# Kernel tuning notes

Hardware: AMD Instinct MI355X
Metric: run time of the kernel (lower is better)

## Reference

```python
import jax, jax.numpy as jnp
import numpy as np

N, H, B = 4096, 128, 32
K_MSG, K_INT = 32, 20
CUTOFFS = (3.0, 3.0, 6.0, 6.0, 10.0, 10.0)  # two EGNN layers per backbone
silu = jax.nn.silu


def _lin(key, fi, fo):
    s = 1.0 / np.sqrt(fi)
    return jax.random.uniform(key, (fi, fo), jnp.float32, -s, s)


def setup_inputs():
    ks = jax.random.split(jax.random.key(0), 16)
    L = 6

    def stack(k, fi, fo):
        return jnp.stack([_lin(kk, fi, fo) for kk in jax.random.split(k, L)])

    return dict(
        h=jax.random.normal(ks[0], (N, H), jnp.float32),
        pos=3.0 * jax.random.normal(ks[1], (N, 3), jnp.float32),
        batch=jnp.sort(jax.random.randint(ks[2], (N,), 0, B)),
        edge_w1=stack(ks[3], 2 * H + 1, H), edge_b1=jnp.zeros((L, H)),
        edge_w2=stack(ks[4], H, H), edge_b2=jnp.zeros((L, H)),
        coord_w1=stack(ks[5], H, H), coord_b1=jnp.zeros((L, H)),
        coord_w2=stack(ks[6], H, 1),
        node_w1=stack(ks[7], 2 * H, H), node_b1=jnp.zeros((L, H)),
        node_w2=stack(ks[8], H, H), node_b2=jnp.zeros((L, H)),
        fw1=_lin(ks[9], H, 128), fb1=jnp.zeros((128,)),
        fw2=_lin(ks[10], 128, 3), fb2=jnp.zeros((3,)),
        iw=jnp.stack([_lin(kk, 2 * H + 2, 1) for kk in jax.random.split(ks[11], 3)]),
        ib=jnp.zeros((3, 1)),
        cw1=_lin(ks[12], H, 128), cb1=jnp.zeros((128,)),
        cw2=_lin(ks[13], 128, 64), cb2=jnp.zeros((64,)),
        sw=_lin(ks[14], H, 1), sb=jnp.zeros((1,)),
    )


def _neighbors(pos, batch, cutoff, k):
    # radius graph with fixed fan-out: k nearest same-graph neighbors within cutoff
    p = jax.lax.stop_gradient(pos)
    d2 = jnp.sum((p[:, None, :] - p[None, :, :]) ** 2, -1)  # [N,N]
    valid = (batch[:, None] == batch[None, :]) & (~jnp.eye(p.shape[0], dtype=bool)) & (d2 <= cutoff * cutoff)
    neg, idx = jax.lax.top_k(jnp.where(valid, -d2, -jnp.inf), k)
    return idx, neg > -jnp.inf  # [N,k] int, [N,k] bool validity mask


def _egnn_layer(h, pos, idx, mask, ew1, eb1, ew2, eb2, cw1, cb1, cw2, nw1, nb1, nw2, nb2):
    mf = mask[..., None].astype(h.dtype)  # [N,K,1]
    hj = h[idx]                            # [N,K,H] gather
    rel = pos[:, None, :] - pos[idx]       # [N,K,3]
    d2 = jnp.sum(rel * rel, -1, keepdims=True)
    hi = jnp.broadcast_to(h[:, None, :], hj.shape)
    m = silu(jnp.concatenate([hi, hj, d2], -1) @ ew1 + eb1)
    m = silu(m @ ew2 + eb2) * mf           # masked messages [N,K,H]
    c = silu(m @ cw1 + cb1) @ cw2          # per-edge coord weight [N,K,1]
    cnt = jnp.maximum(jnp.sum(mf, 1), 1.0)
    pos = pos + jnp.sum(rel * c * mf, 1) / cnt
    h = h + (silu(jnp.concatenate([h, jnp.sum(m, 1)], -1) @ nw1 + nb1) @ nw2 + nb2)
    return h, pos


def _forward(h, pos, batch, edge_w1, edge_b1, edge_w2, edge_b2, coord_w1, coord_b1, coord_w2,
             node_w1, node_b1, node_w2, node_b2, fw1, fb1, fw2, fb2, iw, ib, cw1, cb1, cw2, cb2, sw, sb):
    idx = mask = None
    for l in range(6):  # short(3.0) x2, medium(6.0) x2, long(10.0) x2
        if l % 2 == 0:
            idx, mask = _neighbors(pos, batch, CUTOFFS[l], K_MSG)
        h, pos = _egnn_layer(h, pos, idx, mask, edge_w1[l], edge_b1[l], edge_w2[l], edge_b2[l],
                             coord_w1[l], coord_b1[l], coord_w2[l],
                             node_w1[l], node_b1[l], node_w2[l], node_b2[l])
    forces = jnp.tanh(h @ fw1 + fb1) @ fw2 + fb2
    # interaction detection: radius graph (r=10, max 20 neighbors)
    iidx, imask = _neighbors(pos, batch, 10.0, K_INT)
    rel = pos[:, None, :] - pos[iidx]
    dist = jnp.sqrt(jnp.sum(rel * rel, -1, keepdims=True) + 1e-12)  # [N,K,1]
    hi = jnp.broadcast_to(h[:, None, :], (h.shape[0], K_INT, h.shape[1]))
    feats = jnp.concatenate([hi, h[iidx], dist, dist / 10.0], -1)  # [N,K,2H+2]
    scores = jax.nn.sigmoid(jnp.einsum('nkf,tfo->tnko', feats, iw) + ib[:, None, None, :])
    scores = scores * imask[None, :, :, None].astype(h.dtype)  # zero padded edges
    conformer = jax.nn.relu(h @ cw1 + cb1) @ cw2 + cb2
    steric = h @ sw + sb
    return h, pos, forces, scores[0], scores[1], scores[2], conformer, steric


def reference(h, pos, batch, edge_w1, edge_b1, edge_w2, edge_b2, coord_w1, coord_b1, coord_w2,
              node_w1, node_b1, node_w2, node_b2, fw1, fb1, fw2, fb2, iw, ib, cw1, cb1, cw2, cb2, sw, sb):
    return _forward(h, pos, batch, edge_w1, edge_b1, edge_w2, edge_b2, coord_w1, coord_b1, coord_w2,
                    node_w1, node_b1, node_w2, node_b2, fw1, fb1, fw2, fb2, iw, ib, cw1, cb1, cw2, cb2, sw, sb)
```

## Files before the change

### kernel.cpp

```cpp
#include <hip/hip_runtime.h>
#include <hip/hip_bf16.h>

#define NN 4096
#define HD 128
#define KE 32
#define KI 20
#define XLD 132
#define PLOF 68

#define OFF_H   0
#define OFF_POS 524288
#define OFF_F   536576
#define OFF_S   548864
#define OFF_C   794624
#define OFF_ST  1056768

typedef unsigned short u16;
typedef unsigned int u32;
typedef unsigned long long u64;
typedef __attribute__((ext_vector_type(8))) short bf16x8;
typedef __attribute__((ext_vector_type(4))) float f32x4;

__device__ __forceinline__ float b2f(u16 u) {
  union { u32 i; float f; } c; c.i = ((u32)u) << 16; return c.f;
}
__device__ __forceinline__ float silu_f(float x) { return x / (1.f + __expf(-x)); }
__device__ __forceinline__ void stout(void* out, int fp32m, size_t i, float v) {
  if (fp32m) ((float*)out)[i] = v;
  else ((__hip_bfloat16*)out)[i] = __float2bfloat16(v);
}
__device__ __forceinline__ u32 f2b(float f) {
  u32 u = __float_as_uint(f);
  return (u + 0x7fffu + ((u >> 16) & 1u)) >> 16;
}
__device__ __forceinline__ void packplane(float a, float b, u32& H, u32& L) {
  asm("v_cvt_pk_bf16_f32 %0, %1, %2" : "=v"(H) : "v"(a), "v"(b));
  float hfa = __uint_as_float(H << 16);
  float hfb = __uint_as_float(H & 0xffff0000u);
  asm("v_cvt_pk_bf16_f32 %0, %1, %2" : "=v"(L) : "v"(a - hfa), "v"(b - hfb));
}

__global__ void probe_dtype(const u16* __restrict__ h, int* __restrict__ flag) {
  if (threadIdx.x == 0) atomicExch(flag, 0);
  __syncthreads();
  int bad = 0;
  for (int i = threadIdx.x; i < 8192; i += 256) {
    float v = b2f(h[i]);
    if (!(v > -1000.f && v < 1000.f)) bad = 1;
  }
  if (bad) atomicOr(flag, 1);
}

struct CvtTable {
  const void* src[25];
  int dstoff[25];
  int cnt[25];
};

__global__ void convert_all(CvtTable tab, float* __restrict__ wsf, const int* __restrict__ flag) {
  const int seg = blockIdx.y;
  const int i = blockIdx.x * 256 + threadIdx.x;
  if (i >= tab.cnt[seg]) return;
  float v;
  if (*flag) v = ((const float*)tab.src[seg])[i];
  else       v = b2f(((const u16*)tab.src[seg])[i]);
  wsf[tab.dstoff[seg] + i] = v;
}

__global__ void pack_weights(const float* __restrict__ wsf, int offEW1, int offEW2, int offCW1,
                             u16* __restrict__ WBP) {
  int tid = blockIdx.x * 256 + threadIdx.x;
  if (tid >= 18 * 32768) return;
  int m = tid >> 15;
  int rix = tid & 32767;
  int layer = m / 3, s = m % 3;
  const float* src;
  if (s == 0)      src = wsf + offEW1 + (size_t)layer * 257 * HD + 128 * HD;
  else if (s == 1) src = wsf + offEW2 + (size_t)layer * HD * HD;
  else             src = wsf + offCW1 + (size_t)layer * HD * HD;
  int jh = rix & 15, lane = (rix >> 4) & 63, ot = (rix >> 10) & 7, kt = rix >> 13;
  int j = jh & 7;
  int f = kt * 32 + (lane >> 4) * 8 + j;
  int o = ot * 16 + (lane & 15);
  float v = src[f * HD + o];
  u32 hb = f2b(v);
  float hf = __uint_as_float(hb << 16);
  u32 lb = f2b(v - hf);
  WBP[tid] = (jh < 8) ? (u16)hb : (u16)lb;
}

__global__ void graph_bounds(const int* __restrict__ batch, int* __restrict__ gstart) {
  int n = blockIdx.x * 256 + threadIdx.x;
  if (n >= NN) return;
  int v = batch[n];
  int pv = (n == 0) ? -1 : batch[n - 1];
  for (int b = pv + 1; b <= v; b++) gstart[b] = n;
  if (n == NN - 1) for (int b = v + 1; b <= 32; b++) gstart[b] = NN;
}

__global__ __launch_bounds__(256) void neigh_kernel(
    const float* __restrict__ pos, const int* __restrict__ batch,
    const int* __restrict__ gstart, int* __restrict__ idx, int* __restrict__ cnt,
    int Ksel, float cut2) {
  const int lane = threadIdx.x & 63;
  const int i = blockIdx.x * 4 + (threadIdx.x >> 6);
  const int b = batch[i];
  const int gs = gstart[b];
  const int ge = gstart[b + 1];
  const int span = ge - gs;
  const float px = pos[i * 3 + 0], py = pos[i * 3 + 1], pz = pos[i * 3 + 2];
  u64 key[16];
#pragma unroll
  for (int tq = 0; tq < 16; tq++) {
    u64 k64 = ~0ull;
    if (tq * 64 < span) {
      int j = gs + tq * 64 + lane;
      if (j < ge && j != i) {
        float dx = px - pos[j * 3 + 0];
        float dy = py - pos[j * 3 + 1];
        float dz = pz - pos[j * 3 + 2];
        float d2 = dx * dx + dy * dy + dz * dz;
        if (d2 <= cut2) k64 = (((u64)__float_as_uint(d2)) << 32) | (u32)j;
      }
    }
    key[tq] = k64;
  }
  u64 thresh = 0;
  int myidx = i;
  int mycnt = 0;
  for (int s = 0; s < Ksel; s++) {
    u64 m = ~0ull;
#pragma unroll
    for (int tq = 0; tq < 16; tq++) {
      if (tq * 64 < span) {
        u64 kk = key[tq];
        if (kk >= thresh && kk < m) m = kk;
      }
    }
    for (int off = 32; off > 0; off >>= 1) {
      u64 o = __shfl_down(m, (unsigned)off, 64);
      if (o < m) m = o;
    }
    m = __shfl(m, 0, 64);
    if (m != ~0ull) {
      if (lane == s) myidx = (int)(m & 0xffffffffu);
      mycnt++;
      thresh = m + 1;
    } else break;
  }
  if (lane < Ksel) idx[i * Ksel + lane] = myidx;
  if (lane == 0) cnt[i] = mycnt;
}

__device__ __forceinline__ void mfma_stageS(const u32* xp_, const u16* __restrict__ WP,
                                            int w, int lane, int nt0, int nt1,
                                            f32x4 acc[4]) {
  const int l16 = lane & 15, q = lane >> 4;
  f32x4 z = {0.f, 0.f, 0.f, 0.f};
  acc[0] = z; acc[1] = z; acc[2] = z; acc[3] = z;
#pragma unroll
  for (int kt = 0; kt < 4; kt++) {
    const u16* wb = WP + (size_t)((kt * 8 + w) * 64 + lane) * 16;
    bf16x8 wh = *(const bf16x8*)(wb);
    bf16x8 wl = *(const bf16x8*)(wb + 8);
#pragma unroll
    for (int Et = 0; Et < 4; Et++) {
      if ((Et < 2) ? (Et < nt0) : (Et - 2 < nt1)) {
        const u32* xr = xp_ + (Et * 16 + l16) * XLD + kt * 16 + q * 4;
        bf16x8 xh = *(const bf16x8*)(xr);
        bf16x8 xl = *(const bf16x8*)(xr + PLOF);
        acc[Et] = __builtin_amdgcn_mfma_f32_16x16x32_bf16(wh, xl, acc[Et], 0, 0, 0);
        acc[Et] = __builtin_amdgcn_mfma_f32_16x16x32_bf16(wl, xh, acc[Et], 0, 0, 0);
        acc[Et] = __builtin_amdgcn_mfma_f32_16x16x32_bf16(wh, xh, acc[Et], 0, 0, 0);
      }
    }
  }
}

__global__ __launch_bounds__(512, 4) void egnn_layer(
    const float* __restrict__ h_in, const float* __restrict__ pos_in,
    float* __restrict__ h_out, float* __restrict__ pos_out,
    const int* __restrict__ idx, const int* __restrict__ cnt,
    const float* __restrict__ ew1, const float* __restrict__ eb1,
    const float* __restrict__ eb2,
    const float* __restrict__ cb1, const float* __restrict__ cw2,
    const float* __restrict__ nw1, const float* __restrict__ nb1,
    const float* __restrict__ nw2, const float* __restrict__ nb2,
    const u16* __restrict__ wbp) {
  __shared__ __align__(16) u32 xp[64 * XLD];
  __shared__ float hi_s[2][HD], hpart_s[2][HD], msum_s[2][HD], u_s[2][HD];
  __shared__ float red_s[512];
  __shared__ float ce_red[64][8];
  __shared__ float rel_s[3][64], d2_s[64], mf_s[64], ce_s[64];
  __shared__ int idx_s[64], cn_s[2];

  const int t = threadIdx.x;
  const int i0 = blockIdx.x * 2;
  const int lane = t & 63;
  const int w = __builtin_amdgcn_readfirstlane(t >> 6);
  const int l16 = lane & 15, q = lane >> 4;

  if (t < 64) idx_s[t] = idx[(size_t)(i0 + (t >> 5)) * KE + (t & 31)];
  else if (t < 66) cn_s[t - 64] = cnt[i0 + (t - 64)];
  if (t >= 256) {
    const int nt = t - 256;
    hi_s[nt >> 7][nt & 127] = h_in[(size_t)(i0 + (nt >> 7)) * HD + (nt & 127)];
  }
  __syncthreads();

  const int nt0 = __builtin_amdgcn_readfirstlane((cn_s[0] + 15) >> 4);
  const int nt1 = __builtin_amdgcn_readfirstlane((cn_s[1] + 15) >> 4);

  if (t < 64) {
    const int nd = t >> 5, ic = i0 + nd;
    const int j = idx_s[t];
    const float rx = pos_in[ic * 3 + 0] - pos_in[j * 3 + 0];
    const float ry = pos_in[ic * 3 + 1] - pos_in[j * 3 + 1];
    const float rz = pos_in[ic * 3 + 2] - pos_in[j * 3 + 2];
    rel_s[0][t] = rx; rel_s[1][t] = ry; rel_s[2][t] = rz;
    d2_s[t] = rx * rx + ry * ry + rz * rz;
    mf_s[t] = ((t & 31) < cn_s[nd]) ? 1.0f : 0.0f;
  }
  {
    const int ge_ = t & 63;
    const int myEt = ge_ >> 4;
    const bool glive = (myEt < 2) ? (myEt < nt0) : (myEt - 2 < nt1);
    if (glive) {
      const int j = idx_s[ge_];
      const int f0 = (t >> 6) * 16;
      const float4* src = (const float4*)(h_in + (size_t)j * HD + f0);
      float4 v0 = src[0], v1 = src[1], v2 = src[2], v3 = src[3];
      u32 H0, L0, H1, L1, H2, L2, H3, L3, H4, L4, H5, L5, H6, L6, H7, L7;
      packplane(v0.x, v0.y, H0, L0); packplane(v0.z, v0.w, H1, L1);
      packplane(v1.x, v1.y, H2, L2); packplane(v1.z, v1.w, H3, L3);
      packplane(v2.x, v2.y, H4, L4); packplane(v2.z, v2.w, H5, L5);
      packplane(v3.x, v3.y, H6, L6); packplane(v3.z, v3.w, H7, L7);
      u32* dh = xp + ge_ * XLD + (f0 >> 1);
      uint4 a; a.x = H0; a.y = H1; a.z = H2; a.w = H3;
      uint4 b; b.x = H4; b.y = H5; b.z = H6; b.w = H7;
      uint4 c; c.x = L0; c.y = L1; c.z = L2; c.w = L3;
      uint4 d; d.x = L4; d.y = L5; d.z = L6; d.w = L7;
      *(uint4*)(dh) = a;            *(uint4*)(dh + 4) = b;
      *(uint4*)(dh + PLOF) = c;     *(uint4*)(dh + PLOF + 4) = d;
    }
  }
  {
    const int oo = t & 127, nd = (t >> 7) & 1, hf = t >> 8;
    const float* hsrc = hi_s[nd];
    float hp = 0.f;
#pragma unroll
    for (int f4 = hf * 16; f4 < hf * 16 + 16; f4++) {
      float4 xv = *(const float4*)(hsrc + f4 * 4);
      hp = fmaf(xv.x, ew1[(f4 * 4 + 0) * HD + oo], hp);
      hp = fmaf(xv.y, ew1[(f4 * 4 + 1) * HD + oo], hp);
      hp = fmaf(xv.z, ew1[(f4 * 4 + 2) * HD + oo], hp);
      hp = fmaf(xv.w, ew1[(f4 * 4 + 3) * HD + oo], hp);
    }
    red_s[t] = hp;
  }
  __syncthreads();
  if (t < 256) hpart_s[t >> 7][t & 127] = red_s[t] + red_s[t + 256] + eb1[t & 127];
  __syncthreads();

  {
    f32x4 acc[4];
    mfma_stageS(xp, wbp, w, lane, nt0, nt1, acc);
    __syncthreads();
    const float4 w24 = *(const float4*)(ew1 + 256 * HD + w * 16 + q * 4);
#pragma unroll
    for (int Et = 0; Et < 4; Et++) {
      if ((Et < 2) ? (Et < nt0) : (Et - 2 < nt1)) {
        const int ee = Et * 16 + l16;
        const float d2e = d2_s[ee];
        const float4 hp4 = *(const float4*)(&hpart_s[Et >> 1][w * 16 + q * 4]);
        float s0 = silu_f(acc[Et][0] + hp4.x + d2e * w24.x);
        float s1 = silu_f(acc[Et][1] + hp4.y + d2e * w24.y);
        float s2 = silu_f(acc[Et][2] + hp4.z + d2e * w24.z);
        float s3 = silu_f(acc[Et][3] + hp4.w + d2e * w24.w);
        u32 H0, L0, H1, L1;
        packplane(s0, s1, H0, L0);
        packplane(s2, s3, H1, L1);
        u32* dst = xp + ee * XLD + w * 8 + q * 2;
        uint2 hh; hh.x = H0; hh.y = H1;
        uint2 ll; ll.x = L0; ll.y = L1;
        *(uint2*)(dst) = hh;
        *(uint2*)(dst + PLOF) = ll;
      }
    }
  }
  __syncthreads();

  {
    f32x4 acc[4];
    mfma_stageS(xp, wbp + 32768, w, lane, nt0, nt1, acc);
    __syncthreads();
    const float4 eb4 = *(const float4*)(eb2 + w * 16 + q * 4);
    float ms0x = 0.f, ms0y = 0.f, ms0z = 0.f, ms0w = 0.f;
    float ms1x = 0.f, ms1y = 0.f, ms1z = 0.f, ms1w = 0.f;
#pragma unroll
    for (int Et = 0; Et < 4; Et++) {
      if ((Et < 2) ? (Et < nt0) : (Et - 2 < nt1)) {
        const int ee = Et * 16 + l16;
        const float mfv = mf_s[ee];
        float m0 = (mfv != 0.f) ? silu_f(acc[Et][0] + eb4.x) : 0.f;
        float m1 = (mfv != 0.f) ? silu_f(acc[Et][1] + eb4.y) : 0.f;
        float m2 = (mfv != 0.f) ? silu_f(acc[Et][2] + eb4.z) : 0.f;
        float m3 = (mfv != 0.f) ? silu_f(acc[Et][3] + eb4.w) : 0.f;
        if (Et < 2) { ms0x += m0; ms0y += m1; ms0z += m2; ms0w += m3; }
        else        { ms1x += m0; ms1y += m1; ms1z += m2; ms1w += m3; }
        u32 H0, L0, H1, L1;
        packplane(m0, m1, H0, L0);
        packplane(m2, m3, H1, L1);
        u32* dst = xp + ee * XLD + w * 8 + q * 2;
        uint2 hh; hh.x = H0; hh.y = H1;
        uint2 ll; ll.x = L0; ll.y = L1;
        *(uint2*)(dst) = hh;
        *(uint2*)(dst + PLOF) = ll;
      }
    }
#define RED16(v) v += __shfl_xor(v, 1); v += __shfl_xor(v, 2); \
                 v += __shfl_xor(v, 4); v += __shfl_xor(v, 8);
    RED16(ms0x) RED16(ms0y) RED16(ms0z) RED16(ms0w)
    RED16(ms1x) RED16(ms1y) RED16(ms1z) RED16(ms1w)
#undef RED16
    if (l16 == 0) {
      float4 a; a.x = ms0x; a.y = ms0y; a.z = ms0z; a.w = ms0w;
      float4 b; b.x = ms1x; b.y = ms1y; b.z = ms1z; b.w = ms1w;
      *(float4*)(&msum_s[0][w * 16 + q * 4]) = a;
      *(float4*)(&msum_s[1][w * 16 + q * 4]) = b;
    }
  }
  __syncthreads();

  {
    f32x4 acc[4];
    mfma_stageS(xp, wbp + 65536, w, lane, nt0, nt1, acc);
    const float4 cb4 = *(const float4*)(cb1 + w * 16 + q * 4);
    const float4 cw4 = *(const float4*)(cw2 + w * 16 + q * 4);
#pragma unroll
    for (int Et = 0; Et < 4; Et++) {
      if ((Et < 2) ? (Et < nt0) : (Et - 2 < nt1)) {
        float p = silu_f(acc[Et][0] + cb4.x) * cw4.x;
        p = fmaf(silu_f(acc[Et][1] + cb4.y), cw4.y, p);
        p = fmaf(silu_f(acc[Et][2] + cb4.z), cw4.z, p);
        p = fmaf(silu_f(acc[Et][3] + cb4.w), cw4.w, p);
        p += __shfl_xor(p, 16);
        p += __shfl_xor(p, 32);
        if (lane < 16) ce_red[Et * 16 + lane][w] = p;
      }
    }
  }
  __syncthreads();
  if (t < 64) {
    float c = 0.f;
#pragma unroll
    for (int wv = 0; wv < 8; wv++) c += ce_red[t][wv];
    ce_s[t] = (mf_s[t] != 0.f) ? c : 0.f;
  }
  __syncthreads();
  if (t < 6) {
    const int nd = t / 3, ax = t - nd * 3, ic = i0 + nd;
    float s = 0.f;
#pragma unroll
    for (int k = 0; k < 32; k++) s = fmaf(rel_s[ax][nd * 32 + k], ce_s[nd * 32 + k], s);
    const float cntf = fmaxf((float)cn_s[nd], 1.f);
    pos_out[ic * 3 + ax] = pos_in[ic * 3 + ax] + s / cntf;
  }
  {
    const int oo = t & 127, nd = (t >> 7) & 1, ph = t >> 8;
    const float* src = ph ? msum_s[nd] : hi_s[nd];
    const float* Wp = nw1 + (size_t)ph * 128 * HD + oo;
    float p = 0.f;
#pragma unroll
    for (int f4 = 0; f4 < 32; f4++) {
      float4 xv = *(const float4*)(src + f4 * 4);
      p = fmaf(xv.x, Wp[(f4 * 4 + 0) * HD], p);
      p = fmaf(xv.y, Wp[(f4 * 4 + 1) * HD], p);
      p = fmaf(xv.z, Wp[(f4 * 4 + 2) * HD], p);
      p = fmaf(xv.w, Wp[(f4 * 4 + 3) * HD], p);
    }
    red_s[t] = p;
  }
  __syncthreads();
  if (t < 256) u_s[t >> 7][t & 127] = silu_f(red_s[t] + red_s[t + 256] + nb1[t & 127]);
  __syncthreads();
  {
    const int oo = t & 127, nd = (t >> 7) & 1, ph = t >> 8;
    const float* src = u_s[nd] + ph * 64;
    const float* Wp = nw2 + (size_t)ph * 64 * HD + oo;
    float p = 0.f;
#pragma unroll
    for (int f4 = 0; f4 < 16; f4++) {
      float4 xv = *(const float4*)(src + f4 * 4);
      p = fmaf(xv.x, Wp[(f4 * 4 + 0) * HD], p);
      p = fmaf(xv.y, Wp[(f4 * 4 + 1) * HD], p);
      p = fmaf(xv.z, Wp[(f4 * 4 + 2) * HD], p);
      p = fmaf(xv.w, Wp[(f4 * 4 + 3) * HD], p);
    }
    red_s[t] = p;
  }
  __syncthreads();
  if (t < 256) {
    const int nd = t >> 7, oo = t & 127;
    h_out[(size_t)(i0 + nd) * HD + oo] = hi_s[nd][oo] + red_s[t] + red_s[t + 256] + nb2[oo];
  }
}

__global__ __launch_bounds__(256) void heads_kernel(
    const float* __restrict__ h, const float* __restrict__ pos,
    const float* __restrict__ fw1, const float* __restrict__ fb1,
    const float* __restrict__ fw2, const float* __restrict__ fb2,
    const float* __restrict__ cw1g, const float* __restrict__ cb1g,
    const float* __restrict__ cw2g, const float* __restrict__ cb2g,
    const float* __restrict__ sw, const float* __restrict__ sb,
    const float* __restrict__ iw,
    float* __restrict__ At, float* __restrict__ Bt,
    void* __restrict__ out, const int* __restrict__ flag) {
  __shared__ float hi_s[HD], v1[HD], red_s[256];
  const int i = blockIdx.x, t = threadIdx.x;
  const int fm = *flag;
  if (t < HD) hi_s[t] = h[(size_t)i * HD + t];
  __syncthreads();
  const int o = t & 127, ph = t >> 7;
  {
    float p = 0.f;
#pragma unroll 4
    for (int f = ph * 64; f < ph * 64 + 64; f++) p = fmaf(hi_s[f], fw1[f * HD + o], p);
    red_s[t] = p;
  }
  __syncthreads();
  if (t < HD) v1[t] = tanhf(red_s[t] + red_s[t + 128] + fb1[t]);
  __syncthreads();
  if (t < 3) {
    float p = 0.f;
    for (int f = 0; f < HD; f++) p = fmaf(v1[f], fw2[f * 3 + t], p);
    stout(out, fm, OFF_F + (size_t)i * 3 + t, p + fb2[t]);
  }
  __syncthreads();
  {
    float p = 0.f;
#pragma unroll 4
    for (int f = ph * 64; f < ph * 64 + 64; f++) p = fmaf(hi_s[f], cw1g[f * HD + o], p);
    red_s[t] = p;
  }
  __syncthreads();
  if (t < HD) v1[t] = fmaxf(red_s[t] + red_s[t + 128] + cb1g[t], 0.f);
  __syncthreads();
  {
    const int oo = t & 63, pc = t >> 6;
    float p = 0.f;
#pragma unroll 4
    for (int f = pc * 32; f < pc * 32 + 32; f++) p = fmaf(v1[f], cw2g[f * 64 + oo], p);
    red_s[t] = p;
  }
  __syncthreads();
  if (t < 64)
    stout(out, fm, OFF_C + (size_t)i * 64 + t,
          red_s[t] + red_s[t + 64] + red_s[t + 128] + red_s[t + 192] + cb2g[t]);
  __syncthreads();
  if (t < HD) red_s[t] = hi_s[t] * sw[t];
  __syncthreads();
  if (t == 0) {
    float p = 0.f;
    for (int f = 0; f < HD; f++) p += red_s[f];
    stout(out, fm, OFF_ST + (size_t)i, p + sb[0]);
  }
  __syncthreads();
  {
    const int g = t >> 5, l = t & 31;
    float p = 0.f;
    if (g < 6) {
      const int tt = g >> 1, half = g & 1;
#pragma unroll
      for (int r2 = 0; r2 < 4; r2++)
        p = fmaf(hi_s[l * 4 + r2], iw[tt * 258 + half * 128 + l * 4 + r2], p);
    }
    red_s[t] = p;
  }
  __syncthreads();
  if (t < 6) {
    float p = 0.f;
    for (int l = 0; l < 32; l++) p += red_s[t * 32 + l];
    const int tt = t >> 1;
    if ((t & 1) == 0) At[tt * NN + i] = p;
    else Bt[tt * NN + i] = p;
  }
  if (t < HD) stout(out, fm, OFF_H + (size_t)i * HD + t, hi_s[t]);
  if (t >= 128 && t < 131) stout(out, fm, OFF_POS + (size_t)i * 3 + (t - 128), pos[i * 3 + (t - 128)]);
}

__global__ void scores_kernel(const float* __restrict__ pos, const int* __restrict__ idx2,
                              const int* __restrict__ cnt2, const float* __restrict__ At,
                              const float* __restrict__ Bt, const float* __restrict__ iw,
                              const float* __restrict__ ib, void* __restrict__ out,
                              const int* __restrict__ flag) {
  int tid = blockIdx.x * 256 + threadIdx.x;
  if (tid >= 3 * NN * KI) return;
  const int fm = *flag;
  const int tt = tid / (NN * KI);
  const int r = tid % (NN * KI);
  const int n = r / KI;
  const int k = r % KI;
  float v = 0.f;
  if (k < cnt2[n]) {
    int j = idx2[n * KI + k];
    float dx = pos[n * 3 + 0] - pos[j * 3 + 0];
    float dy = pos[n * 3 + 1] - pos[j * 3 + 1];
    float dz = pos[n * 3 + 2] - pos[j * 3 + 2];
    float d2 = dx * dx + dy * dy + dz * dz;
    float dist = sqrtf(d2 + 1e-12f);
    float s = At[tt * NN + n] + Bt[tt * NN + j] + dist * iw[tt * 258 + 256] +
              (dist * 0.1f) * iw[tt * 258 + 257] + ib[tt];
    v = 1.f / (1.f + __expf(-s));
  }
  stout(out, fm, OFF_S + (size_t)tid, v);
}

extern "C" void kernel_launch(void* const* d_in, const int* in_sizes, int n_in,
                              void* d_out, int out_size, void* d_ws, size_t ws_size,
                              hipStream_t stream) {
  (void)in_sizes; (void)n_in; (void)out_size; (void)ws_size;

  float* wsf = (float*)d_ws;
  float* h_a = wsf + 0;
  float* pos_a = wsf + 524288;
  float* h_b = wsf + 536576;
  float* pos_b = wsf + 1060864;
  float* At = wsf + 1073152;
  float* Bt = wsf + 1085440;
  const int W0 = 1097728;

  static const int wcnt[23] = {197376, 768, 98304, 768, 98304, 768, 768,
                               196608, 768, 98304, 768, 16384, 128, 384, 3,
                               774, 3, 16384, 128, 8192, 64, 128, 1};
  int woff[23];
  {
    int o = W0;
    for (int k = 0; k < 23; k++) { woff[k] = o; o += wcnt[k]; }
  }
  const int IOFF = woff[22] + wcnt[22];
  int* ibase = (int*)d_ws;
  int* idx1 = ibase + IOFF;
  int* cnt1 = idx1 + NN * KE;
  int* idx2 = cnt1 + NN;
  int* cnt2 = idx2 + NN * KI;
  int* gstart = cnt2 + NN;
  int* flag = gstart + 33;
  int wboff = (int)((flag + 1) - ibase);
  wboff = (wboff + 3) & ~3;
  u16* WBP = (u16*)(ibase + wboff);

  const float* EW1 = wsf + woff[0];
  const float* EB1 = wsf + woff[1];
  const float* EB2 = wsf + woff[3];
  const float* CB1 = wsf + woff[5];
  const float* CW2 = wsf + woff[6];
  const float* NW1 = wsf + woff[7];
  const float* NB1 = wsf + woff[8];
  const float* NW2 = wsf + woff[9];
  const float* NB2 = wsf + woff[10];
  const float* FW1 = wsf + woff[11];
  const float* FB1 = wsf + woff[12];
  const float* FW2 = wsf + woff[13];
  const float* FB2 = wsf + woff[14];
  const float* IW = wsf + woff[15];
  const float* IB = wsf + woff[16];
  const float* CW1G = wsf + woff[17];
  const float* CB1G = wsf + woff[18];
  const float* CW2G = wsf + woff[19];
  const float* CB2G = wsf + woff[20];
  const float* SW = wsf + woff[21];
  const float* SB = wsf + woff[22];

  probe_dtype<<<1, 256, 0, stream>>>((const u16*)d_in[0], flag);

  CvtTable tab;
  tab.src[0] = d_in[0]; tab.dstoff[0] = 0;       tab.cnt[0] = NN * HD;
  tab.src[1] = d_in[1]; tab.dstoff[1] = 524288;  tab.cnt[1] = NN * 3;
  for (int k = 0; k < 23; k++) {
    tab.src[2 + k] = d_in[3 + k];
    tab.dstoff[2 + k] = woff[k];
    tab.cnt[2 + k] = wcnt[k];
  }
  {
    dim3 g((NN * HD + 255) / 256, 25, 1);
    convert_all<<<g, 256, 0, stream>>>(tab, wsf, flag);
  }
  pack_weights<<<(18 * 32768 + 255) / 256, 256, 0, stream>>>(
      wsf, woff[0], woff[2], woff[4], WBP);

  const int* batch = (const int*)d_in[2];
  graph_bounds<<<NN / 256, 256, 0, stream>>>(batch, gstart);

  const float cut2s[3] = {9.f, 36.f, 100.f};
  float *hin = h_a, *pin = pos_a, *hout = h_b, *pout = pos_b;
  for (int l = 0; l < 6; l++) {
    if ((l & 1) == 0)
      neigh_kernel<<<NN / 4, 256, 0, stream>>>(pin, batch, gstart, idx1, cnt1, KE, cut2s[l >> 1]);
    egnn_layer<<<NN / 2, 512, 0, stream>>>(
        hin, pin, hout, pout, idx1, cnt1,
        EW1 + (size_t)l * 257 * HD, EB1 + (size_t)l * HD,
        EB2 + (size_t)l * HD,
        CB1 + (size_t)l * HD, CW2 + (size_t)l * HD,
        NW1 + (size_t)l * 256 * HD, NB1 + (size_t)l * HD,
        NW2 + (size_t)l * HD * HD, NB2 + (size_t)l * HD,
        WBP + (size_t)l * 3 * 32768);
    float* th = hin; hin = hout; hout = th;
    float* tp = pin; pin = pout; pout = tp;
  }
  neigh_kernel<<<NN / 4, 256, 0, stream>>>(pin, batch, gstart, idx2, cnt2, KI, 100.f);
  heads_kernel<<<NN, 256, 0, stream>>>(hin, pin, FW1, FB1, FW2, FB2, CW1G, CB1G, CW2G, CB2G,
                                       SW, SB, IW, At, Bt, d_out, flag);
  scores_kernel<<<(3 * NN * KI + 255) / 256, 256, 0, stream>>>(
      pin, idx2, cnt2, At, Bt, IW, IB, d_out, flag);
}
```

Before: 860.5 us.

## Split EGNN layer into hpart, edge MFMA, and node MLP kernels

Splits the fused per-layer kernel into three: a node-level kernel that precomputes the h_i projection of the edge MLP, an edge kernel with 256 threads in which each wave computes two output tiles and holds its weight fragments in registers, and a separate node-update MLP kernel that processes 8 nodes per block. The node GEMVs now reuse each weight load across 8 nodes, where before every block reloaded the full weights for only 2 nodes. The cost is extra launches per layer and a round-trip of hpart and msum through global memory.

```diff
diff --git a/kernel.cpp b/kernel.cpp
--- a/kernel.cpp
+++ b/kernel.cpp
@@ -152,46 +152,117 @@
   if (lane == 0) cnt[i] = mycnt;
 }
 
-__device__ __forceinline__ void mfma_stageS(const u32* xp_, const u16* __restrict__ WP,
-                                            int w, int lane, int nt0, int nt1,
-                                            f32x4 acc[4]) {
-  const int l16 = lane & 15, q = lane >> 4;
-  f32x4 z = {0.f, 0.f, 0.f, 0.f};
-  acc[0] = z; acc[1] = z; acc[2] = z; acc[3] = z;
-#pragma unroll
-  for (int kt = 0; kt < 4; kt++) {
-    const u16* wb = WP + (size_t)((kt * 8 + w) * 64 + lane) * 16;
-    bf16x8 wh = *(const bf16x8*)(wb);
-    bf16x8 wl = *(const bf16x8*)(wb + 8);
-#pragma unroll
-    for (int Et = 0; Et < 4; Et++) {
-      if ((Et < 2) ? (Et < nt0) : (Et - 2 < nt1)) {
-        const u32* xr = xp_ + (Et * 16 + l16) * XLD + kt * 16 + q * 4;
-        bf16x8 xh = *(const bf16x8*)(xr);
-        bf16x8 xl = *(const bf16x8*)(xr + PLOF);
-        acc[Et] = __builtin_amdgcn_mfma_f32_16x16x32_bf16(wh, xl, acc[Et], 0, 0, 0);
-        acc[Et] = __builtin_amdgcn_mfma_f32_16x16x32_bf16(wl, xh, acc[Et], 0, 0, 0);
-        acc[Et] = __builtin_amdgcn_mfma_f32_16x16x32_bf16(wh, xh, acc[Et], 0, 0, 0);
-      }
-    }
-  }
-}
-
-__global__ __launch_bounds__(512, 4) void egnn_layer(
-    const float* __restrict__ h_in, const float* __restrict__ pos_in,
-    float* __restrict__ h_out, float* __restrict__ pos_out,
-    const int* __restrict__ idx, const int* __restrict__ cnt,
-    const float* __restrict__ ew1, const float* __restrict__ eb1,
-    const float* __restrict__ eb2,
-    const float* __restrict__ cb1, const float* __restrict__ cw2,
+__global__ __launch_bounds__(256) void hpart_kernel(
+    const float* __restrict__ h, const float* __restrict__ ew1,
+    const float* __restrict__ eb1, float* __restrict__ hpart) {
+  __shared__ float ht[8][HD];
+  const int t = threadIdx.x;
+  const int n0 = blockIdx.x * 8;
+  {
+    const int nd = t >> 5, f = (t & 31) * 4;
+    *(float4*)(&ht[nd][f]) = *(const float4*)(h + (size_t)(n0 + nd) * HD + f);
+  }
+  __syncthreads();
+  const int nd = t >> 5, ob = (t & 31) * 4;
+  float a0 = 0.f, a1 = 0.f, a2 = 0.f, a3 = 0.f;
+  float b0 = 0.f, b1 = 0.f, b2 = 0.f, b3 = 0.f;
+#pragma unroll 4
+  for (int f = 0; f < 64; f++) {
+    const float x = ht[nd][f];
+    const float4 w4 = *(const float4*)(ew1 + (size_t)f * HD + ob);
+    a0 = fmaf(x, w4.x, a0); a1 = fmaf(x, w4.y, a1);
+    a2 = fmaf(x, w4.z, a2); a3 = fmaf(x, w4.w, a3);
+  }
+#pragma unroll 4
+  for (int f = 64; f < 128; f++) {
+    const float x = ht[nd][f];
+    const float4 w4 = *(const float4*)(ew1 + (size_t)f * HD + ob);
+    b0 = fmaf(x, w4.x, b0); b1 = fmaf(x, w4.y, b1);
+    b2 = fmaf(x, w4.z, b2); b3 = fmaf(x, w4.w, b3);
+  }
+  const float4 e4 = *(const float4*)(eb1 + ob);
+  float4 o4;
+  o4.x = a0 + b0 + e4.x; o4.y = a1 + b1 + e4.y;
+  o4.z = a2 + b2 + e4.z; o4.w = a3 + b3 + e4.w;
+  *(float4*)(hpart + (size_t)(n0 + nd) * HD + ob) = o4;
+}
+
+__global__ __launch_bounds__(256) void node_kernel(
+    const float* __restrict__ h_in, const float* __restrict__ msum,
     const float* __restrict__ nw1, const float* __restrict__ nb1,
     const float* __restrict__ nw2, const float* __restrict__ nb2,
-    const u16* __restrict__ wbp) {
+    float* __restrict__ h_out) {
+  __shared__ float ht[8][HD], mt[8][HD], ut[8][HD];
+  const int t = threadIdx.x;
+  const int n0 = blockIdx.x * 8;
+  {
+    const int nd = t >> 5, f = (t & 31) * 4;
+    *(float4*)(&ht[nd][f]) = *(const float4*)(h_in + (size_t)(n0 + nd) * HD + f);
+    *(float4*)(&mt[nd][f]) = *(const float4*)(msum + (size_t)(n0 + nd) * HD + f);
+  }
+  __syncthreads();
+  const int nd = t >> 5, ob = (t & 31) * 4;
+  float p1[4] = {0.f, 0.f, 0.f, 0.f}, p2[4] = {0.f, 0.f, 0.f, 0.f};
+#pragma unroll 4
+  for (int f = 0; f < 128; f++) {
+    const float x = ht[nd][f];
+    const float4 w4 = *(const float4*)(nw1 + (size_t)f * HD + ob);
+    p1[0] = fmaf(x, w4.x, p1[0]); p1[1] = fmaf(x, w4.y, p1[1]);
+    p1[2] = fmaf(x, w4.z, p1[2]); p1[3] = fmaf(x, w4.w, p1[3]);
+  }
+#pragma unroll 4
+  for (int f = 0; f < 128; f++) {
+    const float x = mt[nd][f];
+    const float4 w4 = *(const float4*)(nw1 + (size_t)(128 + f) * HD + ob);
+    p2[0] = fmaf(x, w4.x, p2[0]); p2[1] = fmaf(x, w4.y, p2[1]);
+    p2[2] = fmaf(x, w4.z, p2[2]); p2[3] = fmaf(x, w4.w, p2[3]);
+  }
+  {
+    const float4 b4 = *(const float4*)(nb1 + ob);
+    ut[nd][ob + 0] = silu_f(p1[0] + p2[0] + b4.x);
+    ut[nd][ob + 1] = silu_f(p1[1] + p2[1] + b4.y);
+    ut[nd][ob + 2] = silu_f(p1[2] + p2[2] + b4.z);
+    ut[nd][ob + 3] = silu_f(p1[3] + p2[3] + b4.w);
+  }
+  __syncthreads();
+  float q1[4] = {0.f, 0.f, 0.f, 0.f}, q2[4] = {0.f, 0.f, 0.f, 0.f};
+#pragma unroll 4
+  for (int f = 0; f < 64; f++) {
+    const float x = ut[nd][f];
+    const float4 w4 = *(const float4*)(nw2 + (size_t)f * HD + ob);
+    q1[0] = fmaf(x, w4.x, q1[0]); q1[1] = fmaf(x, w4.y, q1[1]);
+    q1[2] = fmaf(x, w4.z, q1[2]); q1[3] = fmaf(x, w4.w, q1[3]);
+  }
+#pragma unroll 4
+  for (int f = 64; f < 128; f++) {
+    const float x = ut[nd][f];
+    const float4 w4 = *(const float4*)(nw2 + (size_t)f * HD + ob);
+    q2[0] = fmaf(x, w4.x, q2[0]); q2[1] = fmaf(x, w4.y, q2[1]);
+    q2[2] = fmaf(x, w4.z, q2[2]); q2[3] = fmaf(x, w4.w, q2[3]);
+  }
+  {
+    const float4 b4 = *(const float4*)(nb2 + ob);
+    float4 o4;
+    o4.x = ht[nd][ob + 0] + q1[0] + q2[0] + b4.x;
+    o4.y = ht[nd][ob + 1] + q1[1] + q2[1] + b4.y;
+    o4.z = ht[nd][ob + 2] + q1[2] + q2[2] + b4.z;
+    o4.w = ht[nd][ob + 3] + q1[3] + q2[3] + b4.w;
+    *(float4*)(h_out + (size_t)(n0 + nd) * HD + ob) = o4;
+  }
+}
+
+__global__ __launch_bounds__(256, 4) void egnn_edge(
+    const float* __restrict__ h_in, const float* __restrict__ pos_in,
+    float* __restrict__ pos_out,
+    const int* __restrict__ idx, const int* __restrict__ cnt,
+    const float* __restrict__ hpart, const float* __restrict__ ew1d2,
+    const float* __restrict__ eb2, const float* __restrict__ cb1,
+    const float* __restrict__ cw2,
+    float* __restrict__ msum, const u16* __restrict__ wbp) {
   __shared__ __align__(16) u32 xp[64 * XLD];
-  __shared__ float hi_s[2][HD], hpart_s[2][HD], msum_s[2][HD], u_s[2][HD];
-  __shared__ float red_s[512];
-  __shared__ float ce_red[64][8];
+  __shared__ float hp_s[2][HD];
   __shared__ float rel_s[3][64], d2_s[64], mf_s[64], ce_s[64];
+  __shared__ float ce_red[64][9];
   __shared__ int idx_s[64], cn_s[2];
 
   const int t = threadIdx.x;
@@ -202,14 +273,10 @@
 
   if (t < 64) idx_s[t] = idx[(size_t)(i0 + (t >> 5)) * KE + (t & 31)];
   else if (t < 66) cn_s[t - 64] = cnt[i0 + (t - 64)];
-  if (t >= 256) {
-    const int nt = t - 256;
-    hi_s[nt >> 7][nt & 127] = h_in[(size_t)(i0 + (nt >> 7)) * HD + (nt & 127)];
-  }
-  __syncthreads();
-
+  __syncthreads();
   const int nt0 = __builtin_amdgcn_readfirstlane((cn_s[0] + 15) >> 4);
   const int nt1 = __builtin_amdgcn_readfirstlane((cn_s[1] + 15) >> 4);
+#define LIVE(Et) (((Et) < 2) ? ((Et) < nt0) : ((Et) - 2 < nt1))
 
   if (t < 64) {
     const int nd = t >> 5, ic = i0 + nd;
@@ -222,133 +289,182 @@
     mf_s[t] = ((t & 31) < cn_s[nd]) ? 1.0f : 0.0f;
   }
   {
-    const int ge_ = t & 63;
-    const int myEt = ge_ >> 4;
+    const int nd = t >> 7, f = t & 127;
+    hp_s[nd][f] = hpart[(size_t)(i0 + nd) * HD + f];
+  }
+  {
+    const int e = t & 63;
+    const int myEt = e >> 4;
     const bool glive = (myEt < 2) ? (myEt < nt0) : (myEt - 2 < nt1);
     if (glive) {
-      const int j = idx_s[ge_];
-      const int f0 = (t >> 6) * 16;
+      const int j = idx_s[e];
+      const int f0 = (t >> 6) * 32;
       const float4* src = (const float4*)(h_in + (size_t)j * HD + f0);
-      float4 v0 = src[0], v1 = src[1], v2 = src[2], v3 = src[3];
-      u32 H0, L0, H1, L1, H2, L2, H3, L3, H4, L4, H5, L5, H6, L6, H7, L7;
-      packplane(v0.x, v0.y, H0, L0); packplane(v0.z, v0.w, H1, L1);
-      packplane(v1.x, v1.y, H2, L2); packplane(v1.z, v1.w, H3, L3);
-      packplane(v2.x, v2.y, H4, L4); packplane(v2.z, v2.w, H5, L5);
-      packplane(v3.x, v3.y, H6, L6); packplane(v3.z, v3.w, H7, L7);
-      u32* dh = xp + ge_ * XLD + (f0 >> 1);
-      uint4 a; a.x = H0; a.y = H1; a.z = H2; a.w = H3;
-      uint4 b; b.x = H4; b.y = H5; b.z = H6; b.w = H7;
-      uint4 c; c.x = L0; c.y = L1; c.z = L2; c.w = L3;
-      uint4 d; d.x = L4; d.y = L5; d.z = L6; d.w = L7;
-      *(uint4*)(dh) = a;            *(uint4*)(dh + 4) = b;
-      *(uint4*)(dh + PLOF) = c;     *(uint4*)(dh + PLOF + 4) = d;
-    }
-  }
-  {
-    const int oo = t & 127, nd = (t >> 7) & 1, hf = t >> 8;
-    const float* hsrc = hi_s[nd];
-    float hp = 0.f;
 #pragma unroll
-    for (int f4 = hf * 16; f4 < hf * 16 + 16; f4++) {
-      float4 xv = *(const float4*)(hsrc + f4 * 4);
-      hp = fmaf(xv.x, ew1[(f4 * 4 + 0) * HD + oo], hp);
-      hp = fmaf(xv.y, ew1[(f4 * 4 + 1) * HD + oo], hp);
-      hp = fmaf(xv.z, ew1[(f4 * 4 + 2) * HD + oo], hp);
-      hp = fmaf(xv.w, ew1[(f4 * 4 + 3) * HD + oo], hp);
-    }
-    red_s[t] = hp;
-  }
-  __syncthreads();
-  if (t < 256) hpart_s[t >> 7][t & 127] = red_s[t] + red_s[t + 256] + eb1[t & 127];
-  __syncthreads();
-
-  {
-    f32x4 acc[4];
-    mfma_stageS(xp, wbp, w, lane, nt0, nt1, acc);
+      for (int half = 0; half < 2; half++) {
+        float4 v0 = src[half * 4 + 0], v1 = src[half * 4 + 1];
+        float4 v2 = src[half * 4 + 2], v3 = src[half * 4 + 3];
+        u32 H0, L0, H1, L1, H2, L2, H3, L3, H4, L4, H5, L5, H6, L6, H7, L7;
+        packplane(v0.x, v0.y, H0, L0); packplane(v0.z, v0.w, H1, L1);
+        packplane(v1.x, v1.y, H2, L2); packplane(v1.z, v1.w, H3, L3);
+        packplane(v2.x, v2.y, H4, L4); packplane(v2.z, v2.w, H5, L5);
+        packplane(v3.x, v3.y, H6, L6); packplane(v3.z, v3.w, H7, L7);
+        u32* dh = xp + e * XLD + ((f0 + half * 16) >> 1);
+        uint4 a; a.x = H0; a.y = H1; a.z = H2; a.w = H3;
+        uint4 b; b.x = H4; b.y = H5; b.z = H6; b.w = H7;
+        uint4 c; c.x = L0; c.y = L1; c.z = L2; c.w = L3;
+        uint4 d; d.x = L4; d.y = L5; d.z = L6; d.w = L7;
+        *(uint4*)(dh) = a;        *(uint4*)(dh + 4) = b;
+        *(uint4*)(dh + PLOF) = c; *(uint4*)(dh + PLOF + 4) = d;
+      }
+    }
+  }
+  __syncthreads();
+
+#define MFMA_PASS(WPBASE, accA, accB)                                          \
+  {                                                                            \
+    f32x4 z = {0.f, 0.f, 0.f, 0.f};                                            \
+    accA[0] = z; accA[1] = z; accA[2] = z; accA[3] = z;                        \
+    accB[0] = z; accB[1] = z; accB[2] = z; accB[3] = z;                        \
+    bf16x8 whA[4], wlA[4], whB[4], wlB[4];                                     \
+    _Pragma("unroll")                                                          \
+    for (int kt = 0; kt < 4; kt++) {                                           \
+      const u16* wa = (WPBASE) + (size_t)((kt * 8 + w) * 64 + lane) * 16;      \
+      whA[kt] = *(const bf16x8*)(wa); wlA[kt] = *(const bf16x8*)(wa + 8);      \
+      const u16* wb = (WPBASE) + (size_t)((kt * 8 + w + 4) * 64 + lane) * 16;  \
+      whB[kt] = *(const bf16x8*)(wb); wlB[kt] = *(const bf16x8*)(wb + 8);      \
+    }                                                                          \
+    _Pragma("unroll")                                                          \
+    for (int Et = 0; Et < 4; Et++) {                                           \
+      if (LIVE(Et)) {                                                          \
+        _Pragma("unroll")                                                      \
+        for (int kt = 0; kt < 4; kt++) {                                       \
+          const u32* xr = xp + (Et * 16 + l16) * XLD + kt * 16 + q * 4;        \
+          bf16x8 xh = *(const bf16x8*)(xr);                                    \
+          bf16x8 xl = *(const bf16x8*)(xr + PLOF);                             \
+          accA[Et] = __builtin_amdgcn_mfma_f32_16x16x32_bf16(whA[kt], xl, accA[Et], 0, 0, 0); \
+          accA[Et] = __builtin_amdgcn_mfma_f32_16x16x32_bf16(wlA[kt], xh, accA[Et], 0, 0, 0); \
+          accA[Et] = __builtin_amdgcn_mfma_f32_16x16x32_bf16(whA[kt], xh, accA[Et], 0, 0, 0); \
+          accB[Et] = __builtin_amdgcn_mfma_f32_16x16x32_bf16(whB[kt], xl, accB[Et], 0, 0, 0); \
+          accB[Et] = __builtin_amdgcn_mfma_f32_16x16x32_bf16(wlB[kt], xh, accB[Et], 0, 0, 0); \
+          accB[Et] = __builtin_amdgcn_mfma_f32_16x16x32_bf16(whB[kt], xh, accB[Et], 0, 0, 0); \
+        }                                                                      \
+      }                                                                        \
+    }                                                                          \
+  }
+
+  {
+    f32x4 accA[4], accB[4];
+    MFMA_PASS(wbp, accA, accB)
     __syncthreads();
-    const float4 w24 = *(const float4*)(ew1 + 256 * HD + w * 16 + q * 4);
-#pragma unroll
-    for (int Et = 0; Et < 4; Et++) {
-      if ((Et < 2) ? (Et < nt0) : (Et - 2 < nt1)) {
-        const int ee = Et * 16 + l16;
-        const float d2e = d2_s[ee];
-        const float4 hp4 = *(const float4*)(&hpart_s[Et >> 1][w * 16 + q * 4]);
-        float s0 = silu_f(acc[Et][0] + hp4.x + d2e * w24.x);
-        float s1 = silu_f(acc[Et][1] + hp4.y + d2e * w24.y);
-        float s2 = silu_f(acc[Et][2] + hp4.z + d2e * w24.z);
-        float s3 = silu_f(acc[Et][3] + hp4.w + d2e * w24.w);
-        u32 H0, L0, H1, L1;
-        packplane(s0, s1, H0, L0);
-        packplane(s2, s3, H1, L1);
-        u32* dst = xp + ee * XLD + w * 8 + q * 2;
-        uint2 hh; hh.x = H0; hh.y = H1;
-        uint2 ll; ll.x = L0; ll.y = L1;
-        *(uint2*)(dst) = hh;
-        *(uint2*)(dst + PLOF) = ll;
-      }
-    }
-  }
-  __syncthreads();
-
-  {
-    f32x4 acc[4];
-    mfma_stageS(xp, wbp + 32768, w, lane, nt0, nt1, acc);
+#define EPIB(ACC, OT)                                                          \
+    {                                                                          \
+      const int o = (OT) * 16 + q * 4;                                         \
+      const float4 w24 = *(const float4*)(ew1d2 + o);                          \
+      _Pragma("unroll")                                                        \
+      for (int Et = 0; Et < 4; Et++) {                                         \
+        if (LIVE(Et)) {                                                        \
+          const int ee = Et * 16 + l16;                                        \
+          const float d2e = d2_s[ee];                                          \
+          const float4 hp4 = *(const float4*)(&hp_s[Et >> 1][o]);              \
+          float s0 = silu_f(ACC[Et][0] + hp4.x + d2e * w24.x);                 \
+          float s1 = silu_f(ACC[Et][1] + hp4.y + d2e * w24.y);                 \
+          float s2 = silu_f(ACC[Et][2] + hp4.z + d2e * w24.z);                 \
+          float s3 = silu_f(ACC[Et][3] + hp4.w + d2e * w24.w);                 \
+          u32 H0, L0, H1, L1;                                                  \
+          packplane(s0, s1, H0, L0);                                           \
+          packplane(s2, s3, H1, L1);                                           \
+          u32* dst = xp + ee * XLD + (OT) * 8 + q * 2;                         \
+          uint2 hh; hh.x = H0; hh.y = H1;                                      \
+          uint2 ll; ll.x = L0; ll.y = L1;                                      \
+          *(uint2*)(dst) = hh;                                                 \
+          *(uint2*)(dst + PLOF) = ll;                                          \
+        }                                                                      \
+      }                                                                        \
+    }
+    EPIB(accA, w)
+    EPIB(accB, (w + 4))
+#undef EPIB
+  }
+  __syncthreads();
+
+  {
+    f32x4 accA[4], accB[4];
+    MFMA_PASS(wbp + 32768, accA, accB)
     __syncthreads();
-    const float4 eb4 = *(const float4*)(eb2 + w * 16 + q * 4);
-    float ms0x = 0.f, ms0y = 0.f, ms0z = 0.f, ms0w = 0.f;
-    float ms1x = 0.f, ms1y = 0.f, ms1z = 0.f, ms1w = 0.f;
-#pragma unroll
-    for (int Et = 0; Et < 4; Et++) {
-      if ((Et < 2) ? (Et < nt0) : (Et - 2 < nt1)) {
-        const int ee = Et * 16 + l16;
-        const float mfv = mf_s[ee];
-        float m0 = (mfv != 0.f) ? silu_f(acc[Et][0] + eb4.x) : 0.f;
-        float m1 = (mfv != 0.f) ? silu_f(acc[Et][1] + eb4.y) : 0.f;
-        float m2 = (mfv != 0.f) ? silu_f(acc[Et][2] + eb4.z) : 0.f;
-        float m3 = (mfv != 0.f) ? silu_f(acc[Et][3] + eb4.w) : 0.f;
-        if (Et < 2) { ms0x += m0; ms0y += m1; ms0z += m2; ms0w += m3; }
-        else        { ms1x += m0; ms1y += m1; ms1z += m2; ms1w += m3; }
-        u32 H0, L0, H1, L1;
-        packplane(m0, m1, H0, L0);
-        packplane(m2, m3, H1, L1);
-        u32* dst = xp + ee * XLD + w * 8 + q * 2;
-        uint2 hh; hh.x = H0; hh.y = H1;
-        uint2 ll; ll.x = L0; ll.y = L1;
-        *(uint2*)(dst) = hh;
-        *(uint2*)(dst + PLOF) = ll;
-      }
-    }
+    float msA0[4] = {0.f, 0.f, 0.f, 0.f}, msA1[4] = {0.f, 0.f, 0.f, 0.f};
+    float msB0[4] = {0.f, 0.f, 0.f, 0.f}, msB1[4] = {0.f, 0.f, 0.f, 0.f};
+#define EPIC(ACC, OT, MS0, MS1)                                                \
+    {                                                                          \
+      const int o = (OT) * 16 + q * 4;                                         \
+      const float4 eb4 = *(const float4*)(eb2 + o);                            \
+      _Pragma("unroll")                                                        \
+      for (int Et = 0; Et < 4; Et++) {                                         \
+        if (LIVE(Et)) {                                                        \
+          const int ee = Et * 16 + l16;                                        \
+          const float mfv = mf_s[ee];                                          \
+          float m0 = (mfv != 0.f) ? silu_f(ACC[Et][0] + eb4.x) : 0.f;          \
+          float m1 = (mfv != 0.f) ? silu_f(ACC[Et][1] + eb4.y) : 0.f;          \
+          float m2 = (mfv != 0.f) ? silu_f(ACC[Et][2] + eb4.z) : 0.f;          \
+          float m3 = (mfv != 0.f) ? silu_f(ACC[Et][3] + eb4.w) : 0.f;          \
+          if (Et < 2) { MS0[0] += m0; MS0[1] += m1; MS0[2] += m2; MS0[3] += m3; } \
+          else        { MS1[0] += m0; MS1[1] += m1; MS1[2] += m2; MS1[3] += m3; } \
+          u32 H0, L0, H1, L1;                                                  \
+          packplane(m0, m1, H0, L0);                                           \
+          packplane(m2, m3, H1, L1);                                           \
+          u32* dst = xp + ee * XLD + (OT) * 8 + q * 2;                         \
+          uint2 hh; hh.x = H0; hh.y = H1;                                      \
+          uint2 ll; ll.x = L0; ll.y = L1;                                      \
+          *(uint2*)(dst) = hh;                                                 \
+          *(uint2*)(dst + PLOF) = ll;                                          \
+        }                                                                      \
+      }                                                                        \
+    }
+    EPIC(accA, w, msA0, msA1)
+    EPIC(accB, (w + 4), msB0, msB1)
+#undef EPIC
 #define RED16(v) v += __shfl_xor(v, 1); v += __shfl_xor(v, 2); \
                  v += __shfl_xor(v, 4); v += __shfl_xor(v, 8);
-    RED16(ms0x) RED16(ms0y) RED16(ms0z) RED16(ms0w)
-    RED16(ms1x) RED16(ms1y) RED16(ms1z) RED16(ms1w)
+#pragma unroll
+    for (int r = 0; r < 4; r++) { RED16(msA0[r]) RED16(msA1[r]) RED16(msB0[r]) RED16(msB1[r]) }
 #undef RED16
     if (l16 == 0) {
-      float4 a; a.x = ms0x; a.y = ms0y; a.z = ms0z; a.w = ms0w;
-      float4 b; b.x = ms1x; b.y = ms1y; b.z = ms1z; b.w = ms1w;
-      *(float4*)(&msum_s[0][w * 16 + q * 4]) = a;
-      *(float4*)(&msum_s[1][w * 16 + q * 4]) = b;
-    }
-  }
-  __syncthreads();
-
-  {
-    f32x4 acc[4];
-    mfma_stageS(xp, wbp + 65536, w, lane, nt0, nt1, acc);
-    const float4 cb4 = *(const float4*)(cb1 + w * 16 + q * 4);
-    const float4 cw4 = *(const float4*)(cw2 + w * 16 + q * 4);
-#pragma unroll
-    for (int Et = 0; Et < 4; Et++) {
-      if ((Et < 2) ? (Et < nt0) : (Et - 2 < nt1)) {
-        float p = silu_f(acc[Et][0] + cb4.x) * cw4.x;
-        p = fmaf(silu_f(acc[Et][1] + cb4.y), cw4.y, p);
-        p = fmaf(silu_f(acc[Et][2] + cb4.z), cw4.z, p);
-        p = fmaf(silu_f(acc[Et][3] + cb4.w), cw4.w, p);
-        p += __shfl_xor(p, 16);
-        p += __shfl_xor(p, 32);
-        if (lane < 16) ce_red[Et * 16 + lane][w] = p;
-      }
-    }
+      float4 a0; a0.x = msA0[0]; a0.y = msA0[1]; a0.z = msA0[2]; a0.w = msA0[3];
+      float4 a1; a1.x = msA1[0]; a1.y = msA1[1]; a1.z = msA1[2]; a1.w = msA1[3];
+      float4 b0; b0.x = msB0[0]; b0.y = msB0[1]; b0.z = msB0[2]; b0.w = msB0[3];
+      float4 b1; b1.x = msB1[0]; b1.y = msB1[1]; b1.z = msB1[2]; b1.w = msB1[3];
+      *(float4*)(msum + (size_t)i0 * HD + w * 16 + q * 4) = a0;
+      *(float4*)(msum + (size_t)(i0 + 1) * HD + w * 16 + q * 4) = a1;
+      *(float4*)(msum + (size_t)i0 * HD + (w + 4) * 16 + q * 4) = b0;
+      *(float4*)(msum + (size_t)(i0 + 1) * HD + (w + 4) * 16 + q * 4) = b1;
+    }
+  }
+  __syncthreads();
+
+  {
+    f32x4 accA[4], accB[4];
+    MFMA_PASS(wbp + 65536, accA, accB)
+#define EPID(ACC, OT)                                                          \
+    {                                                                          \
+      const int o = (OT) * 16 + q * 4;                                         \
+      const float4 cb4 = *(const float4*)(cb1 + o);                            \
+      const float4 cw4 = *(const float4*)(cw2 + o);                            \
+      _Pragma("unroll")                                                        \
+      for (int Et = 0; Et < 4; Et++) {                                         \
+        if (LIVE(Et)) {                                                        \
+          float p = silu_f(ACC[Et][0] + cb4.x) * cw4.x;                        \
+          p = fmaf(silu_f(ACC[Et][1] + cb4.y), cw4.y, p);                      \
+          p = fmaf(silu_f(ACC[Et][2] + cb4.z), cw4.z, p);                      \
+          p = fmaf(silu_f(ACC[Et][3] + cb4.w), cw4.w, p);                      \
+          p += __shfl_xor(p, 16);                                              \
+          p += __shfl_xor(p, 32);                                              \
+          if (lane < 16) ce_red[Et * 16 + lane][OT] = p;                       \
+        }                                                                      \
+      }                                                                        \
+    }
+    EPID(accA, w)
+    EPID(accB, (w + 4))
+#undef EPID
   }
   __syncthreads();
   if (t < 64) {
@@ -366,44 +482,8 @@
     const float cntf = fmaxf((float)cn_s[nd], 1.f);
     pos_out[ic * 3 + ax] = pos_in[ic * 3 + ax] + s / cntf;
   }
-  {
-    const int oo = t & 127, nd = (t >> 7) & 1, ph = t >> 8;
-    const float* src = ph ? msum_s[nd] : hi_s[nd];
-    const float* Wp = nw1 + (size_t)ph * 128 * HD + oo;
-    float p = 0.f;
-#pragma unroll
-    for (int f4 = 0; f4 < 32; f4++) {
-      float4 xv = *(const float4*)(src + f4 * 4);
-      p = fmaf(xv.x, Wp[(f4 * 4 + 0) * HD], p);
-      p = fmaf(xv.y, Wp[(f4 * 4 + 1) * HD], p);
-      p = fmaf(xv.z, Wp[(f4 * 4 + 2) * HD], p);
-      p = fmaf(xv.w, Wp[(f4 * 4 + 3) * HD], p);
-    }
-    red_s[t] = p;
-  }
-  __syncthreads();
-  if (t < 256) u_s[t >> 7][t & 127] = silu_f(red_s[t] + red_s[t + 256] + nb1[t & 127]);
-  __syncthreads();
-  {
-    const int oo = t & 127, nd = (t >> 7) & 1, ph = t >> 8;
-    const float* src = u_s[nd] + ph * 64;
-    const float* Wp = nw2 + (size_t)ph * 64 * HD + oo;
-    float p = 0.f;
-#pragma unroll
-    for (int f4 = 0; f4 < 16; f4++) {
-      float4 xv = *(const float4*)(src + f4 * 4);
-      p = fmaf(xv.x, Wp[(f4 * 4 + 0) * HD], p);
-      p = fmaf(xv.y, Wp[(f4 * 4 + 1) * HD], p);
-      p = fmaf(xv.z, Wp[(f4 * 4 + 2) * HD], p);
-      p = fmaf(xv.w, Wp[(f4 * 4 + 3) * HD], p);
-    }
-    red_s[t] = p;
-  }
-  __syncthreads();
-  if (t < 256) {
-    const int nd = t >> 7, oo = t & 127;
-    h_out[(size_t)(i0 + nd) * HD + oo] = hi_s[nd][oo] + red_s[t] + red_s[t + 256] + nb2[oo];
-  }
+#undef LIVE
+#undef MFMA_PASS
 }
 
 __global__ __launch_bounds__(256) void heads_kernel(
@@ -549,6 +629,8 @@
   int wboff = (int)((flag + 1) - ibase);
   wboff = (wboff + 3) & ~3;
   u16* WBP = (u16*)(ibase + wboff);
+  float* HPART = wsf + (wboff + 18 * 32768 / 2);
+  float* MSUM = HPART + (size_t)NN * HD;
 
   const float* EW1 = wsf + woff[0];
   const float* EB1 = wsf + woff[1];
@@ -597,14 +679,16 @@
   for (int l = 0; l < 6; l++) {
     if ((l & 1) == 0)
       neigh_kernel<<<NN / 4, 256, 0, stream>>>(pin, batch, gstart, idx1, cnt1, KE, cut2s[l >> 1]);
-    egnn_layer<<<NN / 2, 512, 0, stream>>>(
-        hin, pin, hout, pout, idx1, cnt1,
-        EW1 + (size_t)l * 257 * HD, EB1 + (size_t)l * HD,
-        EB2 + (size_t)l * HD,
-        CB1 + (size_t)l * HD, CW2 + (size_t)l * HD,
+    hpart_kernel<<<NN / 8, 256, 0, stream>>>(hin, EW1 + (size_t)l * 257 * HD,
+                                             EB1 + (size_t)l * HD, HPART);
+    egnn_edge<<<NN / 2, 256, 0, stream>>>(
+        hin, pin, pout, idx1, cnt1, HPART,
+        EW1 + (size_t)l * 257 * HD + 256 * HD,
+        EB2 + (size_t)l * HD, CB1 + (size_t)l * HD, CW2 + (size_t)l * HD,
+        MSUM, WBP + (size_t)l * 3 * 32768);
+    node_kernel<<<NN / 8, 256, 0, stream>>>(hin, MSUM,
         NW1 + (size_t)l * 256 * HD, NB1 + (size_t)l * HD,
-        NW2 + (size_t)l * HD * HD, NB2 + (size_t)l * HD,
-        WBP + (size_t)l * 3 * 32768);
+        NW2 + (size_t)l * HD * HD, NB2 + (size_t)l * HD, hout);
     float* th = hin; hin = hout; hout = th;
     float* tp = pin; pin = pout; pout = tp;
   }
```

Result: slower. 899.1 us (+4.5%).
